# Performance work log

Measured on AMD Instinct MI355X. Metric: run time of the kernel, lower is better.

## Reference

```python
import jax, jax.numpy as jnp
import numpy as np

B, N, DIM, HEADS = 2, 2048, 1024, 16
HD = DIM // HEADS  # 64


def _rope_table(n, hd):
    pos = jnp.arange(n, dtype=jnp.float32)
    inv_freq = 1.0 / (10000.0 ** (jnp.arange(0, hd, 2, dtype=jnp.float32) / hd))
    ang = pos[:, None] * inv_freq[None, :]                 # [n, hd/2]
    return jnp.stack([jnp.cos(ang), jnp.sin(ang)], -1)      # [n, hd/2, 2]


def setup_inputs() -> dict:
    key = jax.random.key(0)
    ks = jax.random.split(key, 5)
    s = 0.02
    return {
        "x": jax.random.normal(ks[0], (B, N, DIM), jnp.float32),
        "rope": _rope_table(N, HD),
        "qkv_w": jax.random.normal(ks[1], (3 * DIM, DIM), jnp.float32) * s,
        "qkv_b": jax.random.normal(ks[2], (3 * DIM,), jnp.float32) * s,
        "proj_w": jax.random.normal(ks[3], (DIM, DIM), jnp.float32) * s,
        "proj_b": jax.random.normal(ks[4], (DIM,), jnp.float32) * s,
    }


def _apply_rotary(t, rope):
    # t: [b, h, n, d]; rope: [n, d/2, 2] holding (cos, sin)
    b, h, n, d = t.shape
    t2 = t.reshape(b, h, n, d // 2, 2)
    x1, x2 = t2[..., 0], t2[..., 1]
    cos, sin = rope[..., 0], rope[..., 1]                    # [n, d/2]
    o1 = x1 * cos - x2 * sin
    o2 = x1 * sin + x2 * cos
    return jnp.stack([o1, o2], -1).reshape(b, h, n, d)


def reference(x, rope, qkv_w, qkv_b, proj_w, proj_b):
    b, n, ch = x.shape
    qkv = x @ qkv_w.T + qkv_b                                # [b, n, 3*dim]
    qkv = qkv.reshape(b, n, 3, HEADS, HD)
    qkv = jnp.transpose(qkv, (2, 0, 3, 1, 4))                # [3, b, h, n, d]
    q, k, v = qkv[0], qkv[1], qkv[2]
    q = _apply_rotary(q, rope)
    k = _apply_rotary(k, rope)
    scale = 1.0 / jnp.sqrt(jnp.float32(HD))
    scores = jnp.einsum('bhqd,bhkd->bhqk', q, k) * scale     # [b, h, n, n]
    attn = jax.nn.softmax(scores, axis=-1)
    o = jnp.einsum('bhqk,bhkd->bhqd', attn, v)               # [b, h, n, d]
    o = jnp.transpose(o, (0, 2, 1, 3)).reshape(b, n, ch)
    return o @ proj_w.T + proj_b
```

## Files before the change

kernel.cpp:

```cpp
#include <hip/hip_runtime.h>
#include <math.h>

#define NB   2
#define SEQ  2048
#define NDIM 1024
#define NH   16
#define HD   64

using bf16x8 = __attribute__((ext_vector_type(8))) short;
using f32x4  = __attribute__((ext_vector_type(4))) float;

__device__ __forceinline__ unsigned short f2bf(float f) {
    union { float f; unsigned int u; } v; v.f = f;
    unsigned int r = v.u + 0x7fffu + ((v.u >> 16) & 1u);
    return (unsigned short)(r >> 16);
}

__global__ __launch_bounds__(256) void cast_bf16_kernel(
    const float* __restrict__ in, unsigned short* __restrict__ out, int n4)
{
    int i = blockIdx.x * 256 + threadIdx.x;
    if (i < n4) {
        float4 f = ((const float4*)in)[i];
        ushort4 u;
        u.x = f2bf(f.x); u.y = f2bf(f.y); u.z = f2bf(f.z); u.w = f2bf(f.w);
        ((ushort4*)out)[i] = u;
    }
}

__global__ __launch_bounds__(256) void qkv_gemm_kernel(
    const unsigned short* __restrict__ A,
    const unsigned short* __restrict__ W,
    const float* __restrict__ bias,
    const float* __restrict__ rope,
    unsigned short* __restrict__ Qw, unsigned short* __restrict__ Kw,
    unsigned short* __restrict__ Vw)
{
    __shared__ __align__(16) unsigned short As[128][40];
    __shared__ __align__(16) unsigned short Ws[128][40];
    const int tid  = threadIdx.x;
    const int lane = tid & 63;
    const int wv   = tid >> 6;
    const int wr   = wv >> 1, wc = wv & 1;
    const int l15  = lane & 15, lg = lane >> 4;
    const int mbase = blockIdx.y * 128, nbase = blockIdx.x * 128;
    const int srow = tid >> 1, shalf = tid & 1;

    f32x4 acc[4][4] = {};

    const unsigned short* ap = &A[(size_t)(mbase + srow) * 1024 + shalf * 16];
    const unsigned short* wp = &W[(size_t)(nbase + srow) * 1024 + shalf * 16];

    for (int k0 = 0; k0 < 1024; k0 += 32) {
        bf16x8 a0 = *(const bf16x8*)(ap + k0);
        bf16x8 a1 = *(const bf16x8*)(ap + k0 + 8);
        bf16x8 w0 = *(const bf16x8*)(wp + k0);
        bf16x8 w1 = *(const bf16x8*)(wp + k0 + 8);
        *(bf16x8*)&As[srow][shalf * 16]     = a0;
        *(bf16x8*)&As[srow][shalf * 16 + 8] = a1;
        *(bf16x8*)&Ws[srow][shalf * 16]     = w0;
        *(bf16x8*)&Ws[srow][shalf * 16 + 8] = w1;
        __syncthreads();
        bf16x8 af[4], bfr[4];
#pragma unroll
        for (int mf = 0; mf < 4; ++mf)
            af[mf] = *(const bf16x8*)&As[wr * 64 + mf * 16 + l15][lg * 8];
#pragma unroll
        for (int nf = 0; nf < 4; ++nf)
            bfr[nf] = *(const bf16x8*)&Ws[wc * 64 + nf * 16 + l15][lg * 8];
#pragma unroll
        for (int mf = 0; mf < 4; ++mf)
#pragma unroll
            for (int nf = 0; nf < 4; ++nf)
                acc[mf][nf] = __builtin_amdgcn_mfma_f32_16x16x32_bf16(
                    af[mf], bfr[nf], acc[mf][nf], 0, 0, 0);
        __syncthreads();
    }

#pragma unroll
    for (int mf = 0; mf < 4; ++mf) {
#pragma unroll
        for (int r = 0; r < 4; ++r) {
            int m   = mbase + wr * 64 + mf * 16 + lg * 4 + r;
            int bb  = m >> 11;
            int tok = m & 2047;
#pragma unroll
            for (int nf = 0; nf < 4; ++nf) {
                int c = nbase + wc * 64 + nf * 16 + l15;
                float val = acc[mf][nf][r] + bias[c];
                float partner = __shfl_xor(val, 1, 64);
                int sel = c >> 10;
                int hh  = (c >> 6) & 15;
                int d   = c & 63;
                float res = val;
                if (sel < 2) {
                    float cs = rope[((size_t)tok * 32 + (d >> 1)) * 2 + 0];
                    float sn = rope[((size_t)tok * 32 + (d >> 1)) * 2 + 1];
                    if (d & 1) res = partner * sn + val * cs;
                    else       res = val * cs - partner * sn;
                }
                if (sel == 0) res *= 0.18033688011112042f;
                unsigned short* dst = (sel == 0) ? Qw : (sel == 1) ? Kw : Vw;
                dst[((size_t)(bb * NH + hh) * SEQ + tok) * HD + d] = f2bf(res);
            }
        }
    }
}

__device__ __forceinline__ void bar_lds() {
    asm volatile("s_waitcnt lgkmcnt(0)" ::: "memory");
    __builtin_amdgcn_s_barrier();
}

__global__ __launch_bounds__(256, 3) void attn_mfma_kernel(
    const unsigned short* __restrict__ Qw, const unsigned short* __restrict__ Kw,
    const unsigned short* __restrict__ Vw, unsigned short* __restrict__ AO)
{
    __shared__ __align__(16) unsigned short Vt[2][64][64];
    __shared__ __align__(16) unsigned short Ps[4][16][64];

    const int tid  = threadIdx.x;
    const int lane = tid & 63;
    const int wq   = tid >> 6;
    const int l15  = lane & 15, lg = lane >> 4;

    const int id = blockIdx.x;
    const int c8 = id & 7;
    const int t_ = id >> 3;
    const int jq = t_ & 31;
    const int pg = t_ >> 5;
    const int p  = pg * 8 + c8;
    const int hh = p & 15, bb = p >> 4;
    const int qbase = jq * 64;

    const unsigned short* Qb = Qw + (size_t)(bb * NH + hh) * SEQ * HD;
    const unsigned short* Kb = Kw + (size_t)(bb * NH + hh) * SEQ * HD;
    const unsigned short* Vb = Vw + (size_t)(bb * NH + hh) * SEQ * HD;

    bf16x8 qf[2];
#pragma unroll
    for (int ks = 0; ks < 2; ++ks)
        qf[ks] = *(const bf16x8*)&Qb[(size_t)(qbase + wq * 16 + l15) * HD + ks * 32 + lg * 8];

    f32x4 o[4] = {};
    float lrow = 0.f;

    const int kp = tid & 31;
    const int dc = tid >> 5;

    bf16x8 ka[8], kb2[8];
    bf16x8 vr0, vr1;

    auto loadK = [&](bf16x8 (&kr)[8], int kt) {
#pragma unroll
        for (int kf = 0; kf < 4; ++kf)
#pragma unroll
            for (int ks = 0; ks < 2; ++ks)
                kr[kf * 2 + ks] = *(const bf16x8*)
                    &Kb[(size_t)(kt + kf * 16 + l15) * HD + ks * 32 + lg * 8];
    };
    auto loadV = [&](int kt) {
        vr0 = *(const bf16x8*)&Vb[(size_t)(kt + 2 * kp) * HD + dc * 8];
        vr1 = *(const bf16x8*)&Vb[(size_t)(kt + 2 * kp + 1) * HD + dc * 8];
    };
    auto writeV = [&](int buf) {
#pragma unroll
        for (int e = 0; e < 8; ++e) {
            int d = dc * 8 + e;
            unsigned int pk = (unsigned int)(unsigned short)vr0[e]
                            | ((unsigned int)(unsigned short)vr1[e] << 16);
            int ob = (kp * 4) ^ ((d & 7) << 4);
            *(unsigned int*)((char*)&Vt[buf][d][0] + ob) = pk;
        }
    };

    loadV(0);
    loadK(ka, 0);
    writeV(0);
    loadV(64);
    bar_lds();

    auto tile = [&](int t, bf16x8 (&kcur)[8], bf16x8 (&knxt)[8], int cur) {
        f32x4 st[4] = {};
#pragma unroll
        for (int kf = 0; kf < 4; ++kf)
#pragma unroll
            for (int ks = 0; ks < 2; ++ks)
                st[kf] = __builtin_amdgcn_mfma_f32_16x16x32_bf16(
                    kcur[kf * 2 + ks], qf[ks], st[kf], 0, 0, 0);

        if (t + 1 < SEQ / 64) loadK(knxt, (t + 1) * 64);

        float rs = 0.f;
#pragma unroll
        for (int kf = 0; kf < 4; ++kf)
#pragma unroll
            for (int r = 0; r < 4; ++r) {
                st[kf][r] = __builtin_amdgcn_exp2f(st[kf][r]);
                rs += st[kf][r];
            }
        rs += __shfl_xor(rs, 16, 64);
        rs += __shfl_xor(rs, 32, 64);
        lrow += rs;

#pragma unroll
        for (int kf = 0; kf < 4; ++kf) {
            ushort4 w;
            w.x = f2bf(st[kf][0]); w.y = f2bf(st[kf][1]);
            w.z = f2bf(st[kf][2]); w.w = f2bf(st[kf][3]);
            int ob = (kf * 32 + lg * 8) ^ ((l15 & 7) << 4);
            *(ushort4*)((char*)&Ps[wq][l15][0] + ob) = w;
        }

#pragma unroll
        for (int df = 0; df < 4; ++df) {
            const int d = df * 16 + l15;
#pragma unroll
            for (int ks = 0; ks < 2; ++ks) {
                int op = (ks * 64 + lg * 16) ^ ((l15 & 7) << 4);
                bf16x8 pf = *(const bf16x8*)((const char*)&Ps[wq][l15][0] + op);
                bf16x8 vf = *(const bf16x8*)((const char*)&Vt[cur][d][0] + op);
                o[df] = __builtin_amdgcn_mfma_f32_16x16x32_bf16(pf, vf, o[df], 0, 0, 0);
            }
        }

        if (t + 1 < SEQ / 64) writeV(cur ^ 1);
        if (t + 2 < SEQ / 64) loadV((t + 2) * 64);
        bar_lds();
    };

    for (int i = 0; i < SEQ / 128; ++i) {
        tile(2 * i,     ka,  kb2, 0);
        tile(2 * i + 1, kb2, ka,  1);
    }

#pragma unroll
    for (int r = 0; r < 4; ++r) {
        float linv = 1.0f / __shfl(lrow, lg * 4 + r, 64);
        int q = qbase + wq * 16 + lg * 4 + r;
#pragma unroll
        for (int df = 0; df < 4; ++df)
            AO[(size_t)(bb * SEQ + q) * NDIM + hh * HD + df * 16 + l15] =
                f2bf(o[df][r] * linv);
    }
}

__global__ __launch_bounds__(256) void proj_gemm_kernel(
    const unsigned short* __restrict__ A,
    const unsigned short* __restrict__ W,
    const float* __restrict__ bias,
    float* __restrict__ out)
{
    __shared__ __align__(16) unsigned short As[128][40];
    __shared__ __align__(16) unsigned short Ws[128][40];
    const int tid  = threadIdx.x;
    const int lane = tid & 63;
    const int wv   = tid >> 6;
    const int wr   = wv >> 1, wc = wv & 1;
    const int l15  = lane & 15, lg = lane >> 4;
    const int mbase = blockIdx.y * 128, nbase = blockIdx.x * 128;
    const int srow = tid >> 1, shalf = tid & 1;

    f32x4 acc[4][4] = {};

    const unsigned short* ap = &A[(size_t)(mbase + srow) * 1024 + shalf * 16];
    const unsigned short* wp = &W[(size_t)(nbase + srow) * 1024 + shalf * 16];

    for (int k0 = 0; k0 < 1024; k0 += 32) {
        bf16x8 a0 = *(const bf16x8*)(ap + k0);
        bf16x8 a1 = *(const bf16x8*)(ap + k0 + 8);
        bf16x8 w0 = *(const bf16x8*)(wp + k0);
        bf16x8 w1 = *(const bf16x8*)(wp + k0 + 8);
        *(bf16x8*)&As[srow][shalf * 16]     = a0;
        *(bf16x8*)&As[srow][shalf * 16 + 8] = a1;
        *(bf16x8*)&Ws[srow][shalf * 16]     = w0;
        *(bf16x8*)&Ws[srow][shalf * 16 + 8] = w1;
        __syncthreads();
        bf16x8 af[4], bfr[4];
#pragma unroll
        for (int mf = 0; mf < 4; ++mf)
            af[mf] = *(const bf16x8*)&As[wr * 64 + mf * 16 + l15][lg * 8];
#pragma unroll
        for (int nf = 0; nf < 4; ++nf)
            bfr[nf] = *(const bf16x8*)&Ws[wc * 64 + nf * 16 + l15][lg * 8];
#pragma unroll
        for (int mf = 0; mf < 4; ++mf)
#pragma unroll
            for (int nf = 0; nf < 4; ++nf)
                acc[mf][nf] = __builtin_amdgcn_mfma_f32_16x16x32_bf16(
                    af[mf], bfr[nf], acc[mf][nf], 0, 0, 0);
        __syncthreads();
    }

#pragma unroll
    for (int mf = 0; mf < 4; ++mf) {
#pragma unroll
        for (int r = 0; r < 4; ++r) {
            int m = mbase + wr * 64 + mf * 16 + lg * 4 + r;
#pragma unroll
            for (int nf = 0; nf < 4; ++nf) {
                int c = nbase + wc * 64 + nf * 16 + l15;
                out[(size_t)m * 1024 + c] = acc[mf][nf][r] + bias[c];
            }
        }
    }
}

extern "C" void kernel_launch(void* const* d_in, const int* in_sizes, int n_in,
                              void* d_out, int out_size, void* d_ws, size_t ws_size,
                              hipStream_t stream)
{
    (void)in_sizes; (void)n_in; (void)out_size; (void)ws_size;
    const float* x      = (const float*)d_in[0];
    const float* rope   = (const float*)d_in[1];
    const float* qkv_w  = (const float*)d_in[2];
    const float* qkv_b  = (const float*)d_in[3];
    const float* proj_w = (const float*)d_in[4];
    const float* proj_b = (const float*)d_in[5];
    float* out = (float*)d_out;

    unsigned short* ws = (unsigned short*)d_ws;
    const size_t M1 = 1024 * 1024;
    unsigned short* xb     = ws;
    unsigned short* qkvwb  = ws + 4 * M1;
    unsigned short* projwb = ws + 7 * M1;
    unsigned short* Qw     = ws + 8 * M1;
    unsigned short* Kw     = ws + 12 * M1;
    unsigned short* Vw     = ws + 16 * M1;
    unsigned short* AO     = ws + 20 * M1;

    cast_bf16_kernel<<<4096, 256, 0, stream>>>(x, xb, 1048576);
    cast_bf16_kernel<<<3072, 256, 0, stream>>>(qkv_w, qkvwb, 786432);
    cast_bf16_kernel<<<1024, 256, 0, stream>>>(proj_w, projwb, 262144);

    qkv_gemm_kernel<<<dim3(24, 32), 256, 0, stream>>>(
        xb, qkvwb, qkv_b, rope, Qw, Kw, Vw);
    attn_mfma_kernel<<<dim3(1024), 256, 0, stream>>>(Qw, Kw, Vw, AO);
    proj_gemm_kernel<<<dim3(8, 32), 256, 0, stream>>>(AO, projwb, proj_b, out);
}
```

Measured before the change: 315.2 us.

## Software-pipeline QK^T one tile ahead and prefetch K two tiles ahead

Restructures the attention inner loop so the QK^T MFMAs for the next key tile are issued while the current tile's exp/P·V work proceeds, with K register loads moved two tiles ahead. This is meant to hide MFMA latency and global load latency behind softmax and PV compute. It also raises the launch-bounds occupancy hint from 3 to 4 blocks per CU, which constrains registers even though double-buffered score accumulators raise register pressure and risk spills.

```diff
diff --git a/kernel.cpp b/kernel.cpp
--- a/kernel.cpp
+++ b/kernel.cpp
@@ -6,6 +6,7 @@
 #define NDIM 1024
 #define NH   16
 #define HD   64
+#define NT   (SEQ / 64)
 
 using bf16x8 = __attribute__((ext_vector_type(8))) short;
 using f32x4  = __attribute__((ext_vector_type(4))) float;
@@ -112,7 +113,7 @@
     __builtin_amdgcn_s_barrier();
 }
 
-__global__ __launch_bounds__(256, 3) void attn_mfma_kernel(
+__global__ __launch_bounds__(256, 4) void attn_mfma_kernel(
     const unsigned short* __restrict__ Qw, const unsigned short* __restrict__ Kw,
     const unsigned short* __restrict__ Vw, unsigned short* __restrict__ AO)
 {
@@ -173,31 +174,33 @@
             *(unsigned int*)((char*)&Vt[buf][d][0] + ob) = pk;
         }
     };
+    auto qkt = [&](f32x4 (&st)[4], bf16x8 (&kr)[8]) {
+#pragma unroll
+        for (int kf = 0; kf < 4; ++kf) {
+            f32x4 z = {0.f, 0.f, 0.f, 0.f};
+            z = __builtin_amdgcn_mfma_f32_16x16x32_bf16(kr[kf * 2 + 0], qf[0], z, 0, 0, 0);
+            st[kf] = __builtin_amdgcn_mfma_f32_16x16x32_bf16(kr[kf * 2 + 1], qf[1], z, 0, 0, 0);
+        }
+    };
 
     loadV(0);
     loadK(ka, 0);
     writeV(0);
     loadV(64);
+    loadK(kb2, 64);
     bar_lds();
-
-    auto tile = [&](int t, bf16x8 (&kcur)[8], bf16x8 (&knxt)[8], int cur) {
-        f32x4 st[4] = {};
+    f32x4 stA[4], stB[4];
+    qkt(stA, ka);
+
+    auto body = [&](int t, f32x4 (&stC)[4], f32x4 (&stN)[4],
+                    bf16x8 (&kUse)[8], bf16x8 (&kLoad)[8], int cur) {
+        float rs = 0.f;
 #pragma unroll
         for (int kf = 0; kf < 4; ++kf)
 #pragma unroll
-            for (int ks = 0; ks < 2; ++ks)
-                st[kf] = __builtin_amdgcn_mfma_f32_16x16x32_bf16(
-                    kcur[kf * 2 + ks], qf[ks], st[kf], 0, 0, 0);
-
-        if (t + 1 < SEQ / 64) loadK(knxt, (t + 1) * 64);
-
-        float rs = 0.f;
-#pragma unroll
-        for (int kf = 0; kf < 4; ++kf)
-#pragma unroll
             for (int r = 0; r < 4; ++r) {
-                st[kf][r] = __builtin_amdgcn_exp2f(st[kf][r]);
-                rs += st[kf][r];
+                stC[kf][r] = __builtin_amdgcn_exp2f(stC[kf][r]);
+                rs += stC[kf][r];
             }
         rs += __shfl_xor(rs, 16, 64);
         rs += __shfl_xor(rs, 32, 64);
@@ -206,11 +209,15 @@
 #pragma unroll
         for (int kf = 0; kf < 4; ++kf) {
             ushort4 w;
-            w.x = f2bf(st[kf][0]); w.y = f2bf(st[kf][1]);
-            w.z = f2bf(st[kf][2]); w.w = f2bf(st[kf][3]);
+            w.x = f2bf(stC[kf][0]); w.y = f2bf(stC[kf][1]);
+            w.z = f2bf(stC[kf][2]); w.w = f2bf(stC[kf][3]);
             int ob = (kf * 32 + lg * 8) ^ ((l15 & 7) << 4);
             *(ushort4*)((char*)&Ps[wq][l15][0] + ob) = w;
         }
+
+        if (t + 1 < NT) qkt(stN, kUse);
+
+        if (t + 2 < NT) loadK(kLoad, (t + 2) * 64);
 
 #pragma unroll
         for (int df = 0; df < 4; ++df) {
@@ -224,14 +231,14 @@
             }
         }
 
-        if (t + 1 < SEQ / 64) writeV(cur ^ 1);
-        if (t + 2 < SEQ / 64) loadV((t + 2) * 64);
+        if (t + 1 < NT) writeV(cur ^ 1);
+        if (t + 2 < NT) loadV((t + 2) * 64);
         bar_lds();
     };
 
-    for (int i = 0; i < SEQ / 128; ++i) {
-        tile(2 * i,     ka,  kb2, 0);
-        tile(2 * i + 1, kb2, ka,  1);
+    for (int i = 0; i < NT / 2; ++i) {
+        body(2 * i,     stA, stB, kb2, ka,  0);
+        body(2 * i + 1, stB, stA, ka,  kb2, 1);
     }
 
 #pragma unroll
```

New measurement: 315.4 us. About the same (+0.1%).
